# Kernel optimization log

Hardware: AMD Instinct MI355X
Metric: run time of the kernel (lower is better)

## Reference

```python
import jax, jax.numpy as jnp
import numpy as np

N_NODES = 100000
D_FEAT = 128
K_NEIGH = 16
N_LAYERS = 2
F_OUT = 128  # features = [128, 128]


def setup_inputs() -> dict:
    key = jax.random.key(0)
    k1, k2, k3 = jax.random.split(key, 3)
    feats = jax.random.normal(k1, (N_NODES, D_FEAT), dtype=jnp.float32)
    # per-layer sampled neighbor indices (fresh sampling each layer, as in the source)
    neigh_idx = jax.random.randint(k2, (N_LAYERS, N_NODES, K_NEIGH), 0, N_NODES, dtype=jnp.int32)
    # Dense kernels: input is concat(self, mean_neighbors) -> 2*D; both layers 256 -> 128
    Ws = jax.random.normal(k3, (N_LAYERS, 2 * D_FEAT, F_OUT), dtype=jnp.float32) * (1.0 / np.sqrt(2 * D_FEAT))
    bs = jnp.zeros((N_LAYERS, F_OUT), dtype=jnp.float32)
    return {"feats": feats, "neigh_idx": neigh_idx, "Ws": Ws, "bs": bs}


def reference(feats, neigh_idx, Ws, bs):
    """GraphSAGE (mean aggregator): per layer, gather sampled neighbors,
    mean-aggregate, concat with self, Dense; relu between layers.
    Returns the last-layer Dense output (pre-relu), matching `new_feats`
    returned by the source module.
    """
    h = feats  # [N, D]
    z = h
    for l in range(Ws.shape[0]):
        neigh = h[neigh_idx[l]]              # [N, K, D] irregular gather
        agg = neigh.mean(axis=1)             # [N, D] mean aggregation
        cat = jnp.concatenate([h, agg], axis=-1)  # [N, 2D]
        z = cat @ Ws[l] + bs[l]              # [N, F]
        h = jax.nn.relu(z)
    return z
```

## Files before the change

### kernel.cpp

```cpp
#include <hip/hip_runtime.h>

#define N_NODES 100000
#define D 128
#define K 16
#define CATK 256
#define MB 32
#define PAD 8
#define LDSW (CATK + PAD)
#define ZW 132

typedef __attribute__((ext_vector_type(8))) short bf16x8;
typedef __attribute__((ext_vector_type(4))) float f32x4;
typedef __attribute__((ext_vector_type(2))) float f32x2;

__device__ __forceinline__ unsigned short f2bf(float f) {
    union { float f; unsigned u; } v; v.f = f;
    unsigned u = v.u;
    return (unsigned short)((u + 0x7fffu + ((u >> 16) & 1u)) >> 16);
}

__device__ __forceinline__ unsigned pk4(float a, float b, float c, float d) {
    int w = __builtin_amdgcn_cvt_pk_fp8_f32(a, b, 0, false);
    w = __builtin_amdgcn_cvt_pk_fp8_f32(c, d, w, true);
    return (unsigned)w;
}

__device__ __forceinline__ void dec4(unsigned w, float* acc) {
    f32x2 lo = __builtin_amdgcn_cvt_pk_f32_fp8((int)w, false);
    f32x2 hi = __builtin_amdgcn_cvt_pk_f32_fp8((int)w, true);
    acc[0] += lo.x; acc[1] += lo.y; acc[2] += hi.x; acc[3] += hi.y;
}

__global__ void cvt_all(const float* __restrict__ feats, const float* __restrict__ Ws,
                        unsigned* __restrict__ f8, unsigned short* __restrict__ Wt) {
    int tid = blockIdx.x * 256 + threadIdx.x;
    int i = tid * 16;
    if (i < N_NODES * D) {
        const float4* p = (const float4*)(feats + i);
        float4 v0 = p[0], v1 = p[1], v2 = p[2], v3 = p[3];
        uint4 o;
        o.x = pk4(v0.x, v0.y, v0.z, v0.w);
        o.y = pk4(v1.x, v1.y, v1.z, v1.w);
        o.z = pk4(v2.x, v2.y, v2.z, v2.w);
        o.w = pk4(v3.x, v3.y, v3.z, v3.w);
        *(uint4*)(f8 + i / 4) = o;
    }
    if (tid < 2 * CATK * D) {
        int l = tid / (CATK * D);
        int r = tid % (CATK * D);
        int n = r / CATK, k = r % CATK;
        Wt[tid] = f2bf(Ws[l * CATK * D + k * D + n]);
    }
}

template <int LAYER>
__launch_bounds__(256)
__global__ void sage_layer(const float* __restrict__ self_f32,
                           const unsigned short* __restrict__ self_bf,
                           const unsigned char* __restrict__ g8,
                           const int* __restrict__ idx,
                           const unsigned short* __restrict__ Wt,
                           const float* __restrict__ bias,
                           unsigned short* __restrict__ h_out,
                           unsigned char* __restrict__ h8_out,
                           float* __restrict__ z_out) {
    __shared__ __align__(16) char smraw[MB * LDSW * 2];
    unsigned short (*cat)[LDSW] = (unsigned short (*)[LDSW])smraw;
    float (*zb)[ZW] = (float (*)[ZW])smraw;
    __shared__ int sIdx[MB][K];

    const int t = threadIdx.x;
    const int base = blockIdx.x * MB;
    const int lane = t & 63;
    const int wave = t >> 6;
    const int q = lane >> 4;
    const int nlo = lane & 15;

    if (t < MB * K / 4)
        ((int4*)&sIdx[0][0])[t] = ((const int4*)(idx + base * K))[t];
    __syncthreads();

    {
        const int m = t >> 3;
        const int c = (t & 7) * 16;
        const int node = base + m;

        if (LAYER == 0) {
            const float4* sp = (const float4*)(self_f32 + (size_t)node * D + c);
            float sv[16];
            *(f32x4*)&sv[0]  = *(const f32x4*)&sp[0];
            *(f32x4*)&sv[4]  = *(const f32x4*)&sp[1];
            *(f32x4*)&sv[8]  = *(const f32x4*)&sp[2];
            *(f32x4*)&sv[12] = *(const f32x4*)&sp[3];
            unsigned w[8];
#pragma unroll
            for (int j = 0; j < 8; ++j)
                w[j] = (unsigned)f2bf(sv[2 * j]) | ((unsigned)f2bf(sv[2 * j + 1]) << 16);
            *(uint4*)&cat[m][c]     = make_uint4(w[0], w[1], w[2], w[3]);
            *(uint4*)&cat[m][c + 8] = make_uint4(w[4], w[5], w[6], w[7]);
        } else {
            const uint4* sp = (const uint4*)(self_bf + (size_t)node * D + c);
            *(uint4*)&cat[m][c]     = sp[0];
            *(uint4*)&cat[m][c + 8] = sp[1];
        }

        float acc[16];
#pragma unroll
        for (int i = 0; i < 16; ++i) acc[i] = 0.f;
#pragma unroll 4
        for (int k = 0; k < K; ++k) {
            uint4 u = *(const uint4*)(g8 + (size_t)sIdx[m][k] * D + c);
            dec4(u.x, acc + 0);
            dec4(u.y, acc + 4);
            dec4(u.z, acc + 8);
            dec4(u.w, acc + 12);
        }
        unsigned pk[8];
#pragma unroll
        for (int j = 0; j < 8; ++j) {
            unsigned short a = f2bf(acc[2 * j] * (1.f / 16.f));
            unsigned short b = f2bf(acc[2 * j + 1] * (1.f / 16.f));
            pk[j] = (unsigned)a | ((unsigned)b << 16);
        }
        *(uint4*)&cat[m][D + c]     = make_uint4(pk[0], pk[1], pk[2], pk[3]);
        *(uint4*)&cat[m][D + c + 8] = make_uint4(pk[4], pk[5], pk[6], pk[7]);
    }

    bf16x8 bfrag[2][8];
#pragma unroll
    for (int ct = 0; ct < 2; ++ct) {
        int n = wave * 32 + ct * 16 + nlo;
        const unsigned short* wp = Wt + n * CATK + q * 8;
#pragma unroll
        for (int ks = 0; ks < 8; ++ks)
            bfrag[ct][ks] = *(const bf16x8*)(wp + ks * 32);
    }

    __syncthreads();

    f32x4 acc00 = {}, acc01 = {}, acc10 = {}, acc11 = {};
#pragma unroll
    for (int ks = 0; ks < 8; ++ks) {
        bf16x8 a0 = *(const bf16x8*)&cat[nlo][ks * 32 + q * 8];
        bf16x8 a1 = *(const bf16x8*)&cat[16 + nlo][ks * 32 + q * 8];
        acc00 = __builtin_amdgcn_mfma_f32_16x16x32_bf16(a0, bfrag[0][ks], acc00, 0, 0, 0);
        acc01 = __builtin_amdgcn_mfma_f32_16x16x32_bf16(a0, bfrag[1][ks], acc01, 0, 0, 0);
        acc10 = __builtin_amdgcn_mfma_f32_16x16x32_bf16(a1, bfrag[0][ks], acc10, 0, 0, 0);
        acc11 = __builtin_amdgcn_mfma_f32_16x16x32_bf16(a1, bfrag[1][ks], acc11, 0, 0, 0);
    }

    __syncthreads();
#pragma unroll
    for (int ct = 0; ct < 2; ++ct) {
        int col = wave * 32 + ct * 16 + nlo;
        float bv = bias[col];
        f32x4 v0 = (ct == 0) ? acc00 : acc01;
        f32x4 v1 = (ct == 0) ? acc10 : acc11;
#pragma unroll
        for (int r = 0; r < 4; ++r) {
            zb[q * 4 + r][col]      = v0[r] + bv;
            zb[16 + q * 4 + r][col] = v1[r] + bv;
        }
    }
    __syncthreads();
    {
        const int m = t >> 3;
        const int c = (t & 7) * 16;
        float x[16];
        *(f32x4*)&x[0]  = *(const f32x4*)&zb[m][c];
        *(f32x4*)&x[4]  = *(const f32x4*)&zb[m][c + 4];
        *(f32x4*)&x[8]  = *(const f32x4*)&zb[m][c + 8];
        *(f32x4*)&x[12] = *(const f32x4*)&zb[m][c + 12];
        size_t go = (size_t)(base + m) * D + c;
        if (LAYER == 1) {
            float4* zp = (float4*)(z_out + go);
            zp[0] = make_float4(x[0], x[1], x[2], x[3]);
            zp[1] = make_float4(x[4], x[5], x[6], x[7]);
            zp[2] = make_float4(x[8], x[9], x[10], x[11]);
            zp[3] = make_float4(x[12], x[13], x[14], x[15]);
        } else {
#pragma unroll
            for (int i = 0; i < 16; ++i) x[i] = x[i] > 0.f ? x[i] : 0.f;
            unsigned wb[8];
#pragma unroll
            for (int j = 0; j < 8; ++j)
                wb[j] = (unsigned)f2bf(x[2 * j]) | ((unsigned)f2bf(x[2 * j + 1]) << 16);
            uint4* hp = (uint4*)(h_out + go);
            hp[0] = make_uint4(wb[0], wb[1], wb[2], wb[3]);
            hp[1] = make_uint4(wb[4], wb[5], wb[6], wb[7]);
            uint4 o8;
            o8.x = pk4(x[0], x[1], x[2], x[3]);
            o8.y = pk4(x[4], x[5], x[6], x[7]);
            o8.z = pk4(x[8], x[9], x[10], x[11]);
            o8.w = pk4(x[12], x[13], x[14], x[15]);
            *(uint4*)(h8_out + go) = o8;
        }
    }
}

extern "C" void kernel_launch(void* const* d_in, const int* in_sizes, int n_in,
                              void* d_out, int out_size, void* d_ws, size_t ws_size,
                              hipStream_t stream) {
    const float* feats = (const float*)d_in[0];
    const int* neigh   = (const int*)d_in[1];
    const float* Ws    = (const float*)d_in[2];
    const float* bs    = (const float*)d_in[3];
    float* out = (float*)d_out;

    char* ws = (char*)d_ws;
    unsigned short* h1_bf  = (unsigned short*)(ws);
    unsigned char*  feats8 = (unsigned char*)(ws + 25600000);
    unsigned char*  h18    = (unsigned char*)(ws + 38400000);
    unsigned short* Wt     = (unsigned short*)(ws + 51200000);

    cvt_all<<<3125, 256, 0, stream>>>(feats, Ws, (unsigned*)feats8, Wt);

    sage_layer<0><<<N_NODES / MB, 256, 0, stream>>>(
        feats, nullptr, feats8, neigh, Wt, bs, h1_bf, h18, nullptr);
    sage_layer<1><<<N_NODES / MB, 256, 0, stream>>>(
        nullptr, h1_bf, h18, neigh + N_NODES * K, Wt + CATK * D, bs + D,
        nullptr, nullptr, out);
}
```

Baseline: 213.0 us.

## Issue all neighbor gathers up front, drop index LDS staging, direct z store

Measured after the change: 201.2 us. -5.6%, faster.

```diff
diff --git a/kernel.cpp b/kernel.cpp
--- a/kernel.cpp
+++ b/kernel.cpp
@@ -25,10 +25,11 @@
     return (unsigned)w;
 }
 
-__device__ __forceinline__ void dec4(unsigned w, float* acc) {
+__device__ __forceinline__ void dec4p(unsigned w, f32x2* a) {
     f32x2 lo = __builtin_amdgcn_cvt_pk_f32_fp8((int)w, false);
     f32x2 hi = __builtin_amdgcn_cvt_pk_f32_fp8((int)w, true);
-    acc[0] += lo.x; acc[1] += lo.y; acc[2] += hi.x; acc[3] += hi.y;
+    a[0] += lo;
+    a[1] += hi;
 }
 
 __global__ void cvt_all(const float* __restrict__ feats, const float* __restrict__ Ws,
@@ -54,7 +55,7 @@
 }
 
 template <int LAYER>
-__launch_bounds__(256)
+__launch_bounds__(256, 4)
 __global__ void sage_layer(const float* __restrict__ self_f32,
                            const unsigned short* __restrict__ self_bf,
                            const unsigned char* __restrict__ g8,
@@ -67,7 +68,6 @@
     __shared__ __align__(16) char smraw[MB * LDSW * 2];
     unsigned short (*cat)[LDSW] = (unsigned short (*)[LDSW])smraw;
     float (*zb)[ZW] = (float (*)[ZW])smraw;
-    __shared__ int sIdx[MB][K];
 
     const int t = threadIdx.x;
     const int base = blockIdx.x * MB;
@@ -76,22 +76,48 @@
     const int q = lane >> 4;
     const int nlo = lane & 15;
 
-    if (t < MB * K / 4)
-        ((int4*)&sIdx[0][0])[t] = ((const int4*)(idx + base * K))[t];
-    __syncthreads();
-
     {
         const int m = t >> 3;
         const int c = (t & 7) * 16;
         const int node = base + m;
 
+        const int4* ip = (const int4*)(idx + (size_t)node * K);
+        int4 i0 = ip[0], i1 = ip[1], i2 = ip[2], i3 = ip[3];
+
+        float sv[16];
+        uint4 sb0, sb1;
         if (LAYER == 0) {
             const float4* sp = (const float4*)(self_f32 + (size_t)node * D + c);
-            float sv[16];
             *(f32x4*)&sv[0]  = *(const f32x4*)&sp[0];
             *(f32x4*)&sv[4]  = *(const f32x4*)&sp[1];
             *(f32x4*)&sv[8]  = *(const f32x4*)&sp[2];
             *(f32x4*)&sv[12] = *(const f32x4*)&sp[3];
+        } else {
+            const uint4* sp = (const uint4*)(self_bf + (size_t)node * D + c);
+            sb0 = sp[0];
+            sb1 = sp[1];
+        }
+
+        const unsigned char* gp = g8 + c;
+        uint4 u[16];
+        u[0]  = *(const uint4*)(gp + (size_t)i0.x * D);
+        u[1]  = *(const uint4*)(gp + (size_t)i0.y * D);
+        u[2]  = *(const uint4*)(gp + (size_t)i0.z * D);
+        u[3]  = *(const uint4*)(gp + (size_t)i0.w * D);
+        u[4]  = *(const uint4*)(gp + (size_t)i1.x * D);
+        u[5]  = *(const uint4*)(gp + (size_t)i1.y * D);
+        u[6]  = *(const uint4*)(gp + (size_t)i1.z * D);
+        u[7]  = *(const uint4*)(gp + (size_t)i1.w * D);
+        u[8]  = *(const uint4*)(gp + (size_t)i2.x * D);
+        u[9]  = *(const uint4*)(gp + (size_t)i2.y * D);
+        u[10] = *(const uint4*)(gp + (size_t)i2.z * D);
+        u[11] = *(const uint4*)(gp + (size_t)i2.w * D);
+        u[12] = *(const uint4*)(gp + (size_t)i3.x * D);
+        u[13] = *(const uint4*)(gp + (size_t)i3.y * D);
+        u[14] = *(const uint4*)(gp + (size_t)i3.z * D);
+        u[15] = *(const uint4*)(gp + (size_t)i3.w * D);
+
+        if (LAYER == 0) {
             unsigned w[8];
 #pragma unroll
             for (int j = 0; j < 8; ++j)
@@ -99,27 +125,25 @@
             *(uint4*)&cat[m][c]     = make_uint4(w[0], w[1], w[2], w[3]);
             *(uint4*)&cat[m][c + 8] = make_uint4(w[4], w[5], w[6], w[7]);
         } else {
-            const uint4* sp = (const uint4*)(self_bf + (size_t)node * D + c);
-            *(uint4*)&cat[m][c]     = sp[0];
-            *(uint4*)&cat[m][c + 8] = sp[1];
-        }
-
-        float acc[16];
-#pragma unroll
-        for (int i = 0; i < 16; ++i) acc[i] = 0.f;
-#pragma unroll 4
+            *(uint4*)&cat[m][c]     = sb0;
+            *(uint4*)&cat[m][c + 8] = sb1;
+        }
+
+        f32x2 acc2[8];
+#pragma unroll
+        for (int j = 0; j < 8; ++j) acc2[j] = (f32x2){0.f, 0.f};
+#pragma unroll
         for (int k = 0; k < K; ++k) {
-            uint4 u = *(const uint4*)(g8 + (size_t)sIdx[m][k] * D + c);
-            dec4(u.x, acc + 0);
-            dec4(u.y, acc + 4);
-            dec4(u.z, acc + 8);
-            dec4(u.w, acc + 12);
+            dec4p(u[k].x, acc2 + 0);
+            dec4p(u[k].y, acc2 + 2);
+            dec4p(u[k].z, acc2 + 4);
+            dec4p(u[k].w, acc2 + 6);
         }
         unsigned pk[8];
 #pragma unroll
         for (int j = 0; j < 8; ++j) {
-            unsigned short a = f2bf(acc[2 * j] * (1.f / 16.f));
-            unsigned short b = f2bf(acc[2 * j + 1] * (1.f / 16.f));
+            unsigned short a = f2bf(acc2[j].x * (1.f / 16.f));
+            unsigned short b = f2bf(acc2[j].y * (1.f / 16.f));
             pk[j] = (unsigned)a | ((unsigned)b << 16);
         }
         *(uint4*)&cat[m][D + c]     = make_uint4(pk[0], pk[1], pk[2], pk[3]);
@@ -147,6 +171,22 @@
         acc01 = __builtin_amdgcn_mfma_f32_16x16x32_bf16(a0, bfrag[1][ks], acc01, 0, 0, 0);
         acc10 = __builtin_amdgcn_mfma_f32_16x16x32_bf16(a1, bfrag[0][ks], acc10, 0, 0, 0);
         acc11 = __builtin_amdgcn_mfma_f32_16x16x32_bf16(a1, bfrag[1][ks], acc11, 0, 0, 0);
+    }
+
+    if (LAYER == 1) {
+#pragma unroll
+        for (int ct = 0; ct < 2; ++ct) {
+            int col = wave * 32 + ct * 16 + nlo;
+            float bv = bias[col];
+            f32x4 v0 = (ct == 0) ? acc00 : acc01;
+            f32x4 v1 = (ct == 0) ? acc10 : acc11;
+#pragma unroll
+            for (int r = 0; r < 4; ++r) {
+                z_out[(size_t)(base + q * 4 + r) * D + col]      = v0[r] + bv;
+                z_out[(size_t)(base + 16 + q * 4 + r) * D + col] = v1[r] + bv;
+            }
+        }
+        return;
     }
 
     __syncthreads();
@@ -172,29 +212,21 @@
         *(f32x4*)&x[8]  = *(const f32x4*)&zb[m][c + 8];
         *(f32x4*)&x[12] = *(const f32x4*)&zb[m][c + 12];
         size_t go = (size_t)(base + m) * D + c;
-        if (LAYER == 1) {
-            float4* zp = (float4*)(z_out + go);
-            zp[0] = make_float4(x[0], x[1], x[2], x[3]);
-            zp[1] = make_float4(x[4], x[5], x[6], x[7]);
-            zp[2] = make_float4(x[8], x[9], x[10], x[11]);
-            zp[3] = make_float4(x[12], x[13], x[14], x[15]);
-        } else {
-#pragma unroll
-            for (int i = 0; i < 16; ++i) x[i] = x[i] > 0.f ? x[i] : 0.f;
-            unsigned wb[8];
-#pragma unroll
-            for (int j = 0; j < 8; ++j)
-                wb[j] = (unsigned)f2bf(x[2 * j]) | ((unsigned)f2bf(x[2 * j + 1]) << 16);
-            uint4* hp = (uint4*)(h_out + go);
-            hp[0] = make_uint4(wb[0], wb[1], wb[2], wb[3]);
-            hp[1] = make_uint4(wb[4], wb[5], wb[6], wb[7]);
-            uint4 o8;
-            o8.x = pk4(x[0], x[1], x[2], x[3]);
-            o8.y = pk4(x[4], x[5], x[6], x[7]);
-            o8.z = pk4(x[8], x[9], x[10], x[11]);
-            o8.w = pk4(x[12], x[13], x[14], x[15]);
-            *(uint4*)(h8_out + go) = o8;
-        }
+#pragma unroll
+        for (int i = 0; i < 16; ++i) x[i] = x[i] > 0.f ? x[i] : 0.f;
+        unsigned wb[8];
+#pragma unroll
+        for (int j = 0; j < 8; ++j)
+            wb[j] = (unsigned)f2bf(x[2 * j]) | ((unsigned)f2bf(x[2 * j + 1]) << 16);
+        uint4* hp = (uint4*)(h_out + go);
+        hp[0] = make_uint4(wb[0], wb[1], wb[2], wb[3]);
+        hp[1] = make_uint4(wb[4], wb[5], wb[6], wb[7]);
+        uint4 o8;
+        o8.x = pk4(x[0], x[1], x[2], x[3]);
+        o8.y = pk4(x[4], x[5], x[6], x[7]);
+        o8.z = pk4(x[8], x[9], x[10], x[11]);
+        o8.w = pk4(x[12], x[13], x[14], x[15]);
+        *(uint4*)(h8_out + go) = o8;
     }
 }
 
```
